# Performance work log

Measured on AMD Instinct MI355X. Metric: run time of the kernel, lower is better.

## Reference

```python
import jax, jax.numpy as jnp
import numpy as np

K_NEIGHBORS = 6
MAX_NODES = 196
CROP = 64
EVENT_THRESH = 0.1
DIST_THRESH = 4.05 / 4.2  # crop_limit / r_distortion


def _dog_kernel(k, sigma_center, sigma_surround):
    c = k // 2
    y, x = np.meshgrid(np.arange(k, dtype=np.float32), np.arange(k, dtype=np.float32), indexing='ij')
    d2 = (x - c) ** 2 + (y - c) ** 2
    gc = np.exp(-d2 / (2 * sigma_center ** 2)) / (2 * np.pi * sigma_center ** 2)
    gs = np.exp(-d2 / (2 * sigma_surround ** 2)) / (2 * np.pi * sigma_surround ** 2)
    dog = gc - gs
    dog = dog - dog.mean()
    return jnp.asarray(dog, jnp.float32)[None, None]  # [1,1,k,k]


def setup_inputs() -> dict:
    key = jax.random.key(0)
    image = jax.random.normal(key, (64, 3, 512, 512), dtype=jnp.float32)
    return {
        'image': image,
        'w1': _dog_kernel(3, 0.5, 1.0),
        'w2': _dog_kernel(5, 1.0, 2.0),
        'w3': _dog_kernel(9, 2.0, 4.0),
    }


def _crop64(image):
    # F.affine_grid(scale-only theta, 64x64, align_corners=False) + bilinear grid_sample (zero pad)
    B, C, H, W = image.shape
    scale = 16.0 / H
    base = (jnp.arange(CROP, dtype=jnp.float32) + 0.5) / (CROP / 2.0) - 1.0  # (2j+1)/64 - 1
    gx = base * scale
    gy = base * scale
    px = (gx + 1.0) * W / 2.0 - 0.5
    py = (gy + 1.0) * H / 2.0 - 0.5

    def gather_axis(arr, p, size, axis):
        i0 = jnp.floor(p).astype(jnp.int32)
        f = p - i0.astype(p.dtype)
        i1 = i0 + 1
        v0 = ((i0 >= 0) & (i0 < size)).astype(arr.dtype)
        v1 = ((i1 >= 0) & (i1 < size)).astype(arr.dtype)
        a0 = jnp.take(arr, jnp.clip(i0, 0, size - 1), axis=axis)
        a1 = jnp.take(arr, jnp.clip(i1, 0, size - 1), axis=axis)
        sh = [1] * arr.ndim
        sh[axis] = -1
        return a0 * ((1.0 - f) * v0).reshape(sh) + a1 * (f * v1).reshape(sh)

    t = gather_axis(image, px, W, 3)   # [B,C,H,64]
    return gather_axis(t, py, H, 2)    # [B,C,64,64]


def _conv(x, w):
    return jax.lax.conv_general_dilated(x, w, (1, 1), 'SAME', dimension_numbers=('NCHW', 'OIHW', 'NCHW'))


def _safe_sqrt(s2):
    pos = s2 > 0
    return jnp.where(pos, jnp.sqrt(jnp.where(pos, s2, 1.0)), 0.0)


def _forward(image, w1, w2, w3):
    B = image.shape[0]
    crop = _crop64(image)
    gray = crop.mean(axis=1, keepdims=True)  # [B,1,64,64]
    resp = jnp.concatenate([_conv(gray, w1), _conv(gray, w2), _conv(gray, w3)], axis=1)  # [B,3,64,64]

    flat = resp.reshape(B, -1)                       # [B, 3*64*64]
    mag = jnp.abs(flat)
    score = jnp.where(mag > EVENT_THRESH, mag, -1.0)
    vals, idx = jax.lax.top_k(score, MAX_NODES)      # top MAX_NODES events by |response|
    node_valid = vals > EVENT_THRESH                 # [B,N]

    c = idx // (CROP * CROP)
    rem = idx % (CROP * CROP)
    yi = rem // CROP
    xi = rem % CROP
    xc = xi.astype(jnp.float32) / 63.0 * 2.0 - 1.0
    yc = yi.astype(jnp.float32) / 63.0 * 2.0 - 1.0
    ecc = jnp.sqrt(xc ** 2 + yc ** 2)
    rv = jnp.take_along_axis(flat, idx, axis=1)
    pol = jnp.sign(rv)
    nodes = jnp.stack([xc, yc, pol, c.astype(jnp.float32), ecc], axis=-1)  # [B,N,5]
    nodes = nodes * node_valid[..., None].astype(nodes.dtype)

    coords = nodes[..., :2]                          # [B,N,2]
    diff = coords[:, :, None, :] - coords[:, None, :, :]
    dist = _safe_sqrt(jnp.sum(diff ** 2, axis=-1))   # [B,N,N]
    eye = jnp.eye(MAX_NODES, dtype=bool)
    pair_ok = node_valid[:, :, None] & node_valid[:, None, :] & (~eye)[None]
    BIG = jnp.float32(1e9)
    dmask = jnp.where(pair_ok, dist, BIG)
    neg, nbr = jax.lax.top_k(-dmask, K_NEIGHBORS)    # k smallest distances, ascending
    dists = -neg                                     # [B,N,k]
    edge_valid = (dists < DIST_THRESH) & node_valid[:, :, None]

    offs = (jnp.arange(B, dtype=nbr.dtype) * MAX_NODES)[:, None, None]
    src_local = jnp.broadcast_to(jnp.arange(MAX_NODES, dtype=nbr.dtype)[None, :, None], nbr.shape)
    src_g = jnp.where(edge_valid, src_local + offs, 0)
    dst_g = jnp.where(edge_valid, nbr + offs, 0)

    nbr_f = nbr.reshape(B, -1)                                   # [B, N*k]
    dst_xy = jnp.take_along_axis(coords, nbr_f[..., None], axis=1)  # [B,N*k,2]
    src_xy = jnp.repeat(coords, K_NEIGHBORS, axis=1)             # [B,N*k,2]
    dxy = dst_xy - src_xy
    cd = _safe_sqrt(jnp.sum(dxy ** 2, axis=-1))
    ef = jnp.concatenate([dxy, cd[..., None]], axis=-1)          # [B,N*k,3]
    ev = edge_valid.reshape(B, -1)
    ef = ef * ev[..., None].astype(ef.dtype)

    nodes_out = nodes.reshape(B * MAX_NODES, 5)
    edge_index = jnp.stack([src_g.reshape(-1), dst_g.reshape(-1)], axis=0)
    edge_feats = ef.reshape(-1, 3)
    batch_idx = jnp.repeat(jnp.arange(B), MAX_NODES)
    return nodes_out, edge_index, edge_feats, batch_idx, node_valid.reshape(-1), ev.reshape(-1)


def reference(image, w1, w2, w3):
    return _forward(image, w1, w2, w3)
```

## Files before the change

### kernel.cpp

```cpp
#include <hip/hip_runtime.h>
#include <stdint.h>

#define BATCH 64
#define IMH 512
#define IMW 512
#define NCH 3
#define NPIX 4096
#define FLAT 12288
#define MAXN 196
#define KNB 6
#define NTOT (BATCH*MAXN)
#define ETOT (NTOT*KNB)

#define OFF_NODES 0
#define OFF_SRC   62720
#define OFF_DST   137984
#define OFF_EF    213248
#define OFF_BI    439040
#define OFF_NV    451584
#define OFF_EV    464128

__global__ void k_crop_conv(const float* __restrict__ img,
                            const float* __restrict__ w1,
                            const float* __restrict__ w2,
                            const float* __restrict__ w3,
                            float* __restrict__ resp)
{
#pragma clang fp contract(off)
    int blk = blockIdx.x;
    int b   = blk >> 4;
    int rs  = (blk & 15) << 2;
    int tid = threadIdx.x;
    __shared__ float gray[12][64];
    __shared__ float wk1[9], wk2[25], wk3[81];
    if (tid < 9)  wk1[tid] = w1[tid];
    if (tid < 25) wk2[tid] = w2[tid];
    if (tid < 81) wk3[tid] = w3[tid];

    const float* ib = img + (size_t)b * NCH * IMH * IMW;
    for (int s = tid; s < 768; s += 256) {
        int r = s >> 6, x = s & 63;
        int y = rs - 4 + r;
        if (y >= 0 && y < 64) {
            float bx = ((float)x + 0.5f) / 32.0f - 1.0f;
            float gx = bx * 0.03125f;
            float px = (gx + 1.0f) * 512.0f / 2.0f - 0.5f;
            float by = ((float)y + 0.5f) / 32.0f - 1.0f;
            float gy = by * 0.03125f;
            float py = (gy + 1.0f) * 512.0f / 2.0f - 0.5f;
            int ix0 = (int)floorf(px); float fx = px - (float)ix0;
            int iy0 = (int)floorf(py); float fy = py - (float)iy0;
            float wx0 = 1.0f - fx, wx1 = fx;
            float wy0 = 1.0f - fy, wy1 = fy;
            float sc[3];
            for (int c = 0; c < 3; c++) {
                const float* cb = ib + (size_t)c * IMH * IMW;
                float a00 = cb[iy0 * IMW + ix0];
                float a01 = cb[iy0 * IMW + ix0 + 1];
                float a10 = cb[(iy0 + 1) * IMW + ix0];
                float a11 = cb[(iy0 + 1) * IMW + ix0 + 1];
                float t0 = a00 * wx0 + a01 * wx1;
                float t1 = a10 * wx0 + a11 * wx1;
                sc[c] = t0 * wy0 + t1 * wy1;
            }
            gray[r][x] = ((sc[0] + sc[1]) + sc[2]) / 3.0f;
        }
    }
    __syncthreads();

    int ly = tid >> 6;
    int y  = rs + ly;
    int x  = tid & 63;
    double a1 = 0.0, a2 = 0.0, a3 = 0.0;
#pragma unroll
    for (int ky = 0; ky < 3; ky++) {
        int yy = y + ky - 1;
        bool yok = (yy >= 0) & (yy < 64);
        int lr = ly + ky + 3;
#pragma unroll
        for (int kx = 0; kx < 3; kx++) {
            int xx = x + kx - 1;
            if (yok && xx >= 0 && xx < 64)
                a1 += (double)gray[lr][xx] * (double)wk1[ky * 3 + kx];
        }
    }
#pragma unroll
    for (int ky = 0; ky < 5; ky++) {
        int yy = y + ky - 2;
        bool yok = (yy >= 0) & (yy < 64);
        int lr = ly + ky + 2;
#pragma unroll
        for (int kx = 0; kx < 5; kx++) {
            int xx = x + kx - 2;
            if (yok && xx >= 0 && xx < 64)
                a2 += (double)gray[lr][xx] * (double)wk2[ky * 5 + kx];
        }
    }
#pragma unroll
    for (int ky = 0; ky < 9; ky++) {
        int yy = y + ky - 4;
        bool yok = (yy >= 0) & (yy < 64);
        int lr = ly + ky;
#pragma unroll
        for (int kx = 0; kx < 9; kx++) {
            int xx = x + kx - 4;
            if (yok && xx >= 0 && xx < 64)
                a3 += (double)gray[lr][xx] * (double)wk3[ky * 9 + kx];
        }
    }
    size_t base = (size_t)b * FLAT;
    int p = (y << 6) | x;
    resp[base + p]            = (float)a1;
    resp[base + NPIX + p]     = (float)a2;
    resp[base + 2 * NPIX + p] = (float)a3;
}

#define NBIN 2048
#define SCAP 2048

__global__ void k_topk(const float* __restrict__ resp,
                       float* __restrict__ topv,
                       int* __restrict__ topi)
{
    int b = blockIdx.x;
    int tid = threadIdx.x;
    __shared__ uint32_t keys[FLAT];
    __shared__ int hist[NBIN];
    __shared__ int ps[256];
    __shared__ int red[256];
    __shared__ unsigned long long sb[SCAP];
    __shared__ int cnt;

    const float* rb = resp + (size_t)b * FLAT;
    for (int j = tid; j < NBIN; j += 256) hist[j] = 0;
    __syncthreads();
    for (int j = tid; j < FLAT; j += 256) {
        float v = rb[j];
        float m = fabsf(v);
        union { float f; uint32_t u; } cv; cv.f = m;
        uint32_t k = (m > 0.1f) ? cv.u : 0u;
        keys[j] = k;
        if (k) atomicAdd(&hist[k >> 20], 1);
    }
    __syncthreads();

    int part = 0;
#pragma unroll
    for (int q = 0; q < 8; q++) part += hist[tid * 8 + q];
    ps[tid] = part;
    __syncthreads();
    for (int off = 1; off < 256; off <<= 1) {
        int v = ps[tid] + ((tid + off < 256) ? ps[tid + off] : 0);
        __syncthreads();
        ps[tid] = v;
        __syncthreads();
    }
    int base = (tid == 255) ? 0 : ps[tid + 1];
    int best = -1;
    int acc = base;
    for (int q = 7; q >= 0; q--) {
        acc += hist[tid * 8 + q];
        if (acc >= MAXN) { best = tid * 8 + q; break; }
    }
    red[tid] = best;
    __syncthreads();
    for (int off = 128; off >= 1; off >>= 1) {
        if (tid < off) { int o = red[tid + off]; if (o > red[tid]) red[tid] = o; }
        __syncthreads();
    }
    int B = red[0] > 0 ? red[0] : 0;
    if (tid == 0) cnt = 0;
    __syncthreads();

    for (int j = tid; j < FLAT; j += 256) {
        uint32_t k = keys[j];
        if (k && (int)(k >> 20) >= B) {
            int p = atomicAdd(&cnt, 1);
            if (p < SCAP)
                sb[p] = ((unsigned long long)k << 32) | (unsigned long long)(0xFFFFFFFFu - (uint32_t)j);
        }
    }
    __syncthreads();
    int n = cnt; if (n > SCAP) n = SCAP;
    for (int i = tid; i < SCAP; i += 256) if (i >= n) sb[i] = 0ULL;
    __syncthreads();

    for (unsigned k = 2; k <= SCAP; k <<= 1) {
        for (unsigned j = k >> 1; j > 0; j >>= 1) {
            for (unsigned i = tid; i < SCAP; i += 256) {
                unsigned l = i ^ j;
                if (l > i) {
                    unsigned long long a = sb[i], c = sb[l];
                    bool up = ((i & k) == 0);
                    if ((up && a < c) || (!up && a > c)) { sb[i] = c; sb[l] = a; }
                }
            }
            __syncthreads();
        }
    }

    if (tid < MAXN) {
        unsigned long long e = sb[tid];
        uint32_t kh = (uint32_t)(e >> 32);
        if (kh) {
            union { uint32_t u; float f; } cv; cv.u = kh;
            topv[b * MAXN + tid] = cv.f;
            topi[b * MAXN + tid] = (int)(0xFFFFFFFFu - (uint32_t)(e & 0xFFFFFFFFu));
        } else {
            topv[b * MAXN + tid] = -1.0f;
            topi[b * MAXN + tid] = 0;
        }
    }
}

__global__ void k_edges(const float* __restrict__ resp,
                        const float* __restrict__ topv,
                        const int* __restrict__ topi,
                        float* __restrict__ out)
{
#pragma clang fp contract(off)
    int b = blockIdx.x;
    int tid = threadIdx.x;
    __shared__ float cx[MAXN], cy[MAXN];
    __shared__ int   vld[MAXN];

    float* o_nodes = out + OFF_NODES;
    float* o_src   = out + OFF_SRC;
    float* o_dst   = out + OFF_DST;
    float* o_ef    = out + OFF_EF;
    float* o_bi    = out + OFF_BI;
    float* o_nv    = out + OFF_NV;
    float* o_ev    = out + OFF_EV;

    if (tid < MAXN) {
        float v  = topv[b * MAXN + tid];
        int   idx = topi[b * MAXN + tid];
        bool  val = v > 0.1f;
        int c   = idx >> 12;
        int rem = idx & 4095;
        int yi  = rem >> 6;
        int xi  = rem & 63;
        float xc = (float)xi / 63.0f * 2.0f - 1.0f;
        float yc = (float)yi / 63.0f * 2.0f - 1.0f;
        float x2 = xc * xc, y2 = yc * yc;
        float ecc = sqrtf(x2 + y2);
        float rvv = resp[(size_t)b * FLAT + idx];
        float pol = (rvv > 0.0f) ? 1.0f : ((rvv < 0.0f) ? -1.0f : 0.0f);
        float m = val ? 1.0f : 0.0f;
        size_t n = (size_t)b * MAXN + tid;
        o_nodes[n * 5 + 0] = xc * m;
        o_nodes[n * 5 + 1] = yc * m;
        o_nodes[n * 5 + 2] = pol * m;
        o_nodes[n * 5 + 3] = (float)c * m;
        o_nodes[n * 5 + 4] = ecc * m;
        o_nv[n] = m;
        o_bi[n] = (float)b;
        cx[tid] = xc * m;
        cy[tid] = yc * m;
        vld[tid] = val ? 1 : 0;
    }
    __syncthreads();

    if (tid < MAXN) {
        int i = tid;
        float bd[KNB]; int bj[KNB];
#pragma unroll
        for (int k = 0; k < KNB; k++) { bd[k] = 3.0e38f; bj[k] = 0; }
        float cxi = cx[i], cyi = cy[i];
        int vi = vld[i];
        for (int j = 0; j < MAXN; j++) {
            float dx = cxi - cx[j];
            float dy = cyi - cy[j];
            float sx = dx * dx;
            float sy = dy * dy;
            float d2 = sx + sy;
            float dist = (d2 > 0.0f) ? sqrtf(d2) : 0.0f;
            bool ok = vi && vld[j] && (i != j);
            float dm = ok ? dist : 1.0e9f;
            if (dm < bd[KNB - 1]) {
                int p = KNB - 1;
                while (p > 0 && dm < bd[p - 1]) {
                    bd[p] = bd[p - 1]; bj[p] = bj[p - 1]; p--;
                }
                bd[p] = dm; bj[p] = j;
            }
        }
        const float DT = (float)(4.05 / 4.2);
#pragma unroll
        for (int k = 0; k < KNB; k++) {
            float d = bd[k]; int j = bj[k];
            bool ev = (d < DT) && vi;
            float m = ev ? 1.0f : 0.0f;
            float dxf = cx[j] - cxi;
            float dyf = cy[j] - cyi;
            float sx = dxf * dxf;
            float sy = dyf * dyf;
            float s2 = sx + sy;
            float cd = (s2 > 0.0f) ? sqrtf(s2) : 0.0f;
            int e = b * (MAXN * KNB) + i * KNB + k;
            o_src[e] = ev ? (float)(i + b * MAXN) : 0.0f;
            o_dst[e] = ev ? (float)(j + b * MAXN) : 0.0f;
            o_ef[3 * e + 0] = dxf * m;
            o_ef[3 * e + 1] = dyf * m;
            o_ef[3 * e + 2] = cd * m;
            o_ev[e] = m;
        }
    }
}

extern "C" void kernel_launch(void* const* d_in, const int* in_sizes, int n_in,
                              void* d_out, int out_size, void* d_ws, size_t ws_size,
                              hipStream_t stream) {
    const float* img = (const float*)d_in[0];
    const float* w1  = (const float*)d_in[1];
    const float* w2  = (const float*)d_in[2];
    const float* w3  = (const float*)d_in[3];

    float* resp = (float*)d_ws;
    float* topv = resp + (size_t)BATCH * FLAT;
    int*   topi = (int*)(topv + NTOT);
    float* out = (float*)d_out;

    k_crop_conv<<<BATCH * 16, 256, 0, stream>>>(img, w1, w2, w3, resp);
    k_topk<<<BATCH, 256, 0, stream>>>(resp, topv, topi);
    k_edges<<<BATCH, 256, 0, stream>>>(resp, topv, topi, out);
}
```

Before: 393.2 us.

## Fuse top-k and edge kernels, replace bitonic sort with rank counting

The top-k and edge-building kernels become one kernel, so the intermediate topv/topi buffers and one launch go away. The 2048-element bitonic sort with its many block barriers is replaced by a rank count: each candidate counts how many keys beat it and, if its rank is under 196, writes its node directly. Rank counting costs O(n^2) shared reads per block, which is cheap when the candidate set from the histogram threshold is small but grows if many candidates pass. Keys are unique because they include the index, so ranks do not collide.

Result: faster. 335.9 us (-14.6%).

```diff
diff --git a/kernel.cpp b/kernel.cpp
--- a/kernel.cpp
+++ b/kernel.cpp
@@ -118,10 +118,10 @@
 #define NBIN 2048
 #define SCAP 2048
 
-__global__ void k_topk(const float* __restrict__ resp,
-                       float* __restrict__ topv,
-                       int* __restrict__ topi)
+__global__ void k_graph(const float* __restrict__ resp,
+                        float* __restrict__ out)
 {
+#pragma clang fp contract(off)
     int b = blockIdx.x;
     int tid = threadIdx.x;
     __shared__ uint32_t keys[FLAT];
@@ -129,10 +129,21 @@
     __shared__ int ps[256];
     __shared__ int red[256];
     __shared__ unsigned long long sb[SCAP];
+    __shared__ float cx[MAXN], cy[MAXN];
+    __shared__ int   vld[MAXN];
     __shared__ int cnt;
+
+    float* o_nodes = out + OFF_NODES;
+    float* o_src   = out + OFF_SRC;
+    float* o_dst   = out + OFF_DST;
+    float* o_ef    = out + OFF_EF;
+    float* o_bi    = out + OFF_BI;
+    float* o_nv    = out + OFF_NV;
+    float* o_ev    = out + OFF_EV;
 
     const float* rb = resp + (size_t)b * FLAT;
     for (int j = tid; j < NBIN; j += 256) hist[j] = 0;
+    if (tid == 0) cnt = 0;
     __syncthreads();
     for (int j = tid; j < FLAT; j += 256) {
         float v = rb[j];
@@ -169,7 +180,6 @@
         __syncthreads();
     }
     int B = red[0] > 0 ? red[0] : 0;
-    if (tid == 0) cnt = 0;
     __syncthreads();
 
     for (int j = tid; j < FLAT; j += 256) {
@@ -182,83 +192,49 @@
     }
     __syncthreads();
     int n = cnt; if (n > SCAP) n = SCAP;
-    for (int i = tid; i < SCAP; i += 256) if (i >= n) sb[i] = 0ULL;
-    __syncthreads();
-
-    for (unsigned k = 2; k <= SCAP; k <<= 1) {
-        for (unsigned j = k >> 1; j > 0; j >>= 1) {
-            for (unsigned i = tid; i < SCAP; i += 256) {
-                unsigned l = i ^ j;
-                if (l > i) {
-                    unsigned long long a = sb[i], c = sb[l];
-                    bool up = ((i & k) == 0);
-                    if ((up && a < c) || (!up && a > c)) { sb[i] = c; sb[l] = a; }
-                }
-            }
-            __syncthreads();
-        }
-    }
-
-    if (tid < MAXN) {
-        unsigned long long e = sb[tid];
-        uint32_t kh = (uint32_t)(e >> 32);
-        if (kh) {
-            union { uint32_t u; float f; } cv; cv.u = kh;
-            topv[b * MAXN + tid] = cv.f;
-            topi[b * MAXN + tid] = (int)(0xFFFFFFFFu - (uint32_t)(e & 0xFFFFFFFFu));
-        } else {
-            topv[b * MAXN + tid] = -1.0f;
-            topi[b * MAXN + tid] = 0;
-        }
-    }
-}
-
-__global__ void k_edges(const float* __restrict__ resp,
-                        const float* __restrict__ topv,
-                        const int* __restrict__ topi,
-                        float* __restrict__ out)
-{
-#pragma clang fp contract(off)
-    int b = blockIdx.x;
-    int tid = threadIdx.x;
-    __shared__ float cx[MAXN], cy[MAXN];
-    __shared__ int   vld[MAXN];
-
-    float* o_nodes = out + OFF_NODES;
-    float* o_src   = out + OFF_SRC;
-    float* o_dst   = out + OFF_DST;
-    float* o_ef    = out + OFF_EF;
-    float* o_bi    = out + OFF_BI;
-    float* o_nv    = out + OFF_NV;
-    float* o_ev    = out + OFF_EV;
-
-    if (tid < MAXN) {
-        float v  = topv[b * MAXN + tid];
-        int   idx = topi[b * MAXN + tid];
-        bool  val = v > 0.1f;
-        int c   = idx >> 12;
-        int rem = idx & 4095;
-        int yi  = rem >> 6;
-        int xi  = rem & 63;
-        float xc = (float)xi / 63.0f * 2.0f - 1.0f;
-        float yc = (float)yi / 63.0f * 2.0f - 1.0f;
-        float x2 = xc * xc, y2 = yc * yc;
-        float ecc = sqrtf(x2 + y2);
-        float rvv = resp[(size_t)b * FLAT + idx];
-        float pol = (rvv > 0.0f) ? 1.0f : ((rvv < 0.0f) ? -1.0f : 0.0f);
-        float m = val ? 1.0f : 0.0f;
-        size_t n = (size_t)b * MAXN + tid;
-        o_nodes[n * 5 + 0] = xc * m;
-        o_nodes[n * 5 + 1] = yc * m;
-        o_nodes[n * 5 + 2] = pol * m;
-        o_nodes[n * 5 + 3] = (float)c * m;
-        o_nodes[n * 5 + 4] = ecc * m;
-        o_nv[n] = m;
-        o_bi[n] = (float)b;
-        cx[tid] = xc * m;
-        cy[tid] = yc * m;
-        vld[tid] = val ? 1 : 0;
-    }
+    int nv = n < MAXN ? n : MAXN;
+
+    for (int e = tid; e < n; e += 256) {
+        unsigned long long key = sb[e];
+        int rank = 0;
+        for (int j = 0; j < n; j++) rank += (sb[j] > key) ? 1 : 0;
+        if (rank < MAXN) {
+            int idx = (int)(0xFFFFFFFFu - (uint32_t)(key & 0xFFFFFFFFu));
+            int c   = idx >> 12;
+            int rem = idx & 4095;
+            int yi  = rem >> 6;
+            int xi  = rem & 63;
+            float xc = (float)xi / 63.0f * 2.0f - 1.0f;
+            float yc = (float)yi / 63.0f * 2.0f - 1.0f;
+            float x2 = xc * xc, y2 = yc * yc;
+            float ecc = sqrtf(x2 + y2);
+            float rvv = rb[idx];
+            float pol = (rvv > 0.0f) ? 1.0f : ((rvv < 0.0f) ? -1.0f : 0.0f);
+            size_t nn = (size_t)b * MAXN + rank;
+            o_nodes[nn * 5 + 0] = xc;
+            o_nodes[nn * 5 + 1] = yc;
+            o_nodes[nn * 5 + 2] = pol;
+            o_nodes[nn * 5 + 3] = (float)c;
+            o_nodes[nn * 5 + 4] = ecc;
+            o_nv[nn] = 1.0f;
+            cx[rank] = xc;
+            cy[rank] = yc;
+            vld[rank] = 1;
+        }
+    }
+    if (tid >= nv && tid < MAXN) {
+        size_t nn = (size_t)b * MAXN + tid;
+        o_nodes[nn * 5 + 0] = 0.0f;
+        o_nodes[nn * 5 + 1] = 0.0f;
+        o_nodes[nn * 5 + 2] = 0.0f;
+        o_nodes[nn * 5 + 3] = 0.0f;
+        o_nodes[nn * 5 + 4] = 0.0f;
+        o_nv[nn] = 0.0f;
+        cx[tid] = 0.0f;
+        cy[tid] = 0.0f;
+        vld[tid] = 0;
+    }
+    if (tid < MAXN) o_bi[(size_t)b * MAXN + tid] = (float)b;
     __syncthreads();
 
     if (tid < MAXN) {
@@ -317,11 +293,8 @@
     const float* w3  = (const float*)d_in[3];
 
     float* resp = (float*)d_ws;
-    float* topv = resp + (size_t)BATCH * FLAT;
-    int*   topi = (int*)(topv + NTOT);
     float* out = (float*)d_out;
 
     k_crop_conv<<<BATCH * 16, 256, 0, stream>>>(img, w1, w2, w3, resp);
-    k_topk<<<BATCH, 256, 0, stream>>>(resp, topv, topi);
-    k_edges<<<BATCH, 256, 0, stream>>>(resp, topv, topi, out);
+    k_graph<<<BATCH, 256, 0, stream>>>(resp, out);
 }
```
